# Kernel tuning notes

Measured on AMD Instinct MI355X. Metric: run time of the kernel, lower is better.

## Reference

```python
import jax, jax.numpy as jnp
import numpy as np

NUM_EMBEDDINGS = 1024
EMBEDDING_DIM = 256
COMMITMENT_COST = 0.25


def setup_inputs() -> dict:
    key = jax.random.key(0)
    kz, kc = jax.random.split(key)
    z = jax.random.normal(kz, (32, 32, 32, EMBEDDING_DIM), dtype=jnp.float32)
    # torch init: uniform(-1/K, 1/K)
    codebook = jax.random.uniform(
        kc, (NUM_EMBEDDINGS, EMBEDDING_DIM), dtype=jnp.float32,
        minval=-1.0 / NUM_EMBEDDINGS, maxval=1.0 / NUM_EMBEDDINGS)
    return {"z": z, "codebook": codebook}


def reference(z, codebook):
    K, D = codebook.shape
    zf = z.reshape(-1, D)                                   # [N, D]
    # squared L2 distances via expansion: ||z||^2 + ||e||^2 - 2 z.e
    distances = (jnp.sum(zf * zf, axis=1, keepdims=True)
                 + jnp.sum(codebook * codebook, axis=1)
                 - 2.0 * jnp.matmul(zf, codebook.T))        # [N, K]
    idx = jnp.argmin(distances, axis=1)                     # [N]
    encodings = jax.nn.one_hot(idx, K, dtype=z.dtype)       # [N, K]
    quantized = jnp.matmul(encodings, codebook).reshape(z.shape)
    e_latent_loss = jnp.mean((jax.lax.stop_gradient(quantized) - z) ** 2)
    q_latent_loss = jnp.mean((quantized - jax.lax.stop_gradient(z)) ** 2)
    loss = q_latent_loss + COMMITMENT_COST * e_latent_loss
    quantized_st = z + jax.lax.stop_gradient(quantized - z)  # straight-through
    return quantized_st, loss, encodings
```

## Files before the change

kernel.cpp:

```cpp
#include <hip/hip_runtime.h>

#define N_ROWS 32768
#define DIM 256
#define K_CODES 1024
#define KTOT 768
#define OUT_QUANT 8388608

typedef unsigned long long ull;
typedef _Float16 f16;
typedef __attribute__((ext_vector_type(4))) _Float16 f16x4;
typedef __attribute__((ext_vector_type(8))) _Float16 f16x8;
typedef __attribute__((ext_vector_type(4))) float f32x4;

#define NB_ZSPLIT 8192
#define NB_ZNORM 2048
#define NB_CSPLIT 256
#define NB_CNORM 64

struct HL { f16 h, l; };
__device__ __forceinline__ HL split2(float x) {
  f16 hh = (f16)x;
  if (__builtin_fabsf(x) < 6.103515625e-05f) hh = (f16)0.0f;
  const float r = __fsub_rn(x, (float)hh);
  HL o;
  o.h = hh;
  o.l = (f16)(__fmul_rn(r, 4096.0f));
  return o;
}

__global__ __launch_bounds__(256) void prep(
    const float* __restrict__ z, const float* __restrict__ cb,
    f16* __restrict__ Ap, f16* __restrict__ Bp,
    float* __restrict__ rn, float* __restrict__ cn,
    ull* __restrict__ keys, float* __restrict__ out) {
  const int b = blockIdx.x, tid = threadIdx.x;
  if (b < NB_ZSPLIT) {
    const size_t g = ((size_t)b * 256 + tid) * 4;
    const int row = (int)(g >> 8), k = (int)(g & 255);
    const float4 v = *(const float4*)(z + g);
    const HL s0 = split2(v.x), s1 = split2(v.y), s2 = split2(v.z), s3 = split2(v.w);
    const f16x4 h = {s0.h, s1.h, s2.h, s3.h};
    const f16x4 l = {s0.l, s1.l, s2.l, s3.l};
    f16* arow = Ap + (size_t)row * KTOT + k;
    *(f16x4*)(arow) = h;
    *(f16x4*)(arow + 256) = l;
    *(f16x4*)(arow + 512) = h;
  } else if (b < NB_ZSPLIT + NB_ZNORM) {
    const int row = (b - NB_ZSPLIT) * 16 + (tid >> 4);
    const int j = tid & 7, half = (tid >> 3) & 1;
    const float* x = z + (size_t)row * DIM + half * 128 + j;
    float r = __fmul_rn(x[0], x[0]);
#pragma unroll
    for (int t = 1; t < 16; ++t) r = __fadd_rn(r, __fmul_rn(x[8 * t], x[8 * t]));
    r = __fadd_rn(r, __shfl_xor(r, 1));
    r = __fadd_rn(r, __shfl_xor(r, 2));
    r = __fadd_rn(r, __shfl_xor(r, 4));
    const float o = __shfl_xor(r, 8);
    if ((tid & 15) == 0) {
      rn[row] = __fadd_rn(r, o);
      keys[row] = ~0ull;
    }
  } else if (b < NB_ZSPLIT + NB_ZNORM + NB_CSPLIT) {
    const int b2 = b - (NB_ZSPLIT + NB_ZNORM);
    const size_t g = ((size_t)b2 * 256 + tid) * 4;
    const int row = (int)(g >> 8), k = (int)(g & 255);
    const float4 v = *(const float4*)(cb + g);
    const HL s0 = split2(__fmul_rn(v.x, 1024.0f));
    const HL s1 = split2(__fmul_rn(v.y, 1024.0f));
    const HL s2 = split2(__fmul_rn(v.z, 1024.0f));
    const HL s3 = split2(__fmul_rn(v.w, 1024.0f));
    const f16x4 h = {s0.h, s1.h, s2.h, s3.h};
    const f16x4 l = {s0.l, s1.l, s2.l, s3.l};
    f16* brow = Bp + (size_t)row * KTOT + k;
    *(f16x4*)(brow) = h;
    *(f16x4*)(brow + 256) = h;
    *(f16x4*)(brow + 512) = l;
    if (b2 == 0 && tid == 0) out[OUT_QUANT] = 0.0f;
  } else {
    const int row = (b - (NB_ZSPLIT + NB_ZNORM + NB_CSPLIT)) * 16 + (tid >> 4);
    const int j = tid & 7, half = (tid >> 3) & 1;
    const float* x = cb + (size_t)row * DIM + half * 128 + j;
    float r = __fmul_rn(x[0], x[0]);
#pragma unroll
    for (int t = 1; t < 16; ++t) r = __fadd_rn(r, __fmul_rn(x[8 * t], x[8 * t]));
    r = __fadd_rn(r, __shfl_xor(r, 1));
    r = __fadd_rn(r, __shfl_xor(r, 2));
    r = __fadd_rn(r, __shfl_xor(r, 4));
    const float o = __shfl_xor(r, 8);
    if ((tid & 15) == 0) cn[row] = __fadd_rn(r, o);
  }
}

__device__ __forceinline__ void lds16(const void* g, void* l) {
  __builtin_amdgcn_global_load_lds(
      (const __attribute__((address_space(1))) unsigned int*)g,
      (__attribute__((address_space(3))) unsigned int*)l, 16, 0, 0);
}

__device__ __forceinline__ ull shflx64(ull v, int m) {
  int lo = __shfl_xor((int)(v & 0xffffffffull), m);
  int hi = __shfl_xor((int)(v >> 32), m);
  return ((ull)(unsigned int)hi << 32) | (unsigned int)lo;
}

__global__ __launch_bounds__(256) void gemm_argmin_f16(
    const f16* __restrict__ Ap, const f16* __restrict__ Bp,
    const float* __restrict__ rn, const float* __restrict__ cn,
    ull* __restrict__ keys) {
  __shared__ f16 As[2][4096];
  __shared__ f16 Bs[2][4096];

  const int bid = blockIdx.x;
  const int xcd = bid & 7, ii = bid >> 3;
  const int bm = xcd * 32 + (ii >> 3), bn = ii & 7;
  const int row0 = bm * 128, col0 = bn * 128;
  const int tid = threadIdx.x, wid = tid >> 6, lane = tid & 63;
  const int wm = wid >> 1, wn = wid & 1, lq = lane >> 4, lr = lane & 15;
  const int srow = tid & 127, shalf = tid >> 7;

  f32x4 acc[4][4];
#pragma unroll
  for (int a = 0; a < 4; ++a)
#pragma unroll
    for (int c = 0; c < 4; ++c) acc[a][c] = (f32x4){0.f, 0.f, 0.f, 0.f};

  const f16* aG = Ap + (size_t)(row0 + srow) * KTOT + shalf * 8;
  const f16* bG = Bp + (size_t)(col0 + srow) * KTOT + shalf * 8;

#pragma unroll
  for (int is = 0; is < 2; ++is) {
    lds16(aG + is * 16, (char*)As[0] + is * 4096 + tid * 16);
    lds16(bG + is * 16, (char*)Bs[0] + is * 4096 + tid * 16);
  }
  __syncthreads();

#pragma unroll
  for (int t = 0; t < 24; ++t) {
    const int cur = t & 1, nxt = cur ^ 1;
    if (t < 23) {
#pragma unroll
      for (int is = 0; is < 2; ++is) {
        lds16(aG + (t + 1) * 32 + is * 16, (char*)As[nxt] + is * 4096 + tid * 16);
        lds16(bG + (t + 1) * 32 + is * 16, (char*)Bs[nxt] + is * 4096 + tid * 16);
      }
    }
    if (t == 8) {
#pragma unroll
      for (int a = 0; a < 4; ++a)
#pragma unroll
        for (int c = 0; c < 4; ++c) acc[a][c] *= 4096.0f;
    }
    f16x8 av[4], bv[4];
    const f16x8* As8 = (const f16x8*)As[cur];
    const f16x8* Bs8 = (const f16x8*)Bs[cur];
#pragma unroll
    for (int fm = 0; fm < 4; ++fm) av[fm] = As8[lq * 128 + wm * 64 + fm * 16 + lr];
#pragma unroll
    for (int fn = 0; fn < 4; ++fn) bv[fn] = Bs8[lq * 128 + wn * 64 + fn * 16 + lr];
#pragma unroll
    for (int fm = 0; fm < 4; ++fm)
#pragma unroll
      for (int fn = 0; fn < 4; ++fn)
        acc[fm][fn] = __builtin_amdgcn_mfma_f32_16x16x32_f16(av[fm], bv[fn],
                                                             acc[fm][fn], 0, 0, 0);
    __syncthreads();
  }

  float cnv[4];
#pragma unroll
  for (int fn = 0; fn < 4; ++fn) cnv[fn] = cn[col0 + wn * 64 + fn * 16 + lr];

#pragma unroll
  for (int fm = 0; fm < 4; ++fm) {
#pragma unroll
    for (int j = 0; j < 4; ++j) {
      const int rg = row0 + wm * 64 + fm * 16 + lq * 4 + j;
      const float a_rn = rn[rg];
      ull best = ~0ull;
#pragma unroll
      for (int fn = 0; fn < 4; ++fn) {
        const int cg = col0 + wn * 64 + fn * 16 + lr;
        const float d = __fsub_rn(__fadd_rn(a_rn, cnv[fn]),
                                  __fmul_rn(acc[fm][fn][j], 4.76837158203125e-07f));
        unsigned int mono = __float_as_uint(d);
        mono = (mono & 0x80000000u) ? ~mono : (mono | 0x80000000u);
        const ull key = ((ull)mono << 32) | (unsigned int)cg;
        if (key < best) best = key;
      }
#pragma unroll
      for (int off = 1; off <= 8; off <<= 1) {
        ull o = shflx64(best, off);
        if (o < best) best = o;
      }
      if (lr == 0) atomicMin(&keys[rg], best);
    }
  }
}

__global__ __launch_bounds__(256) void quantize_out(
    const float* __restrict__ z, const float* __restrict__ cb,
    const ull* __restrict__ keys, float* __restrict__ out) {
  __shared__ float ls[4];
  const int wid = threadIdx.x >> 6, lane = threadIdx.x & 63;
  const int row = blockIdx.x * 4 + wid;
  const int idx = (int)(keys[row] & 0xffffffffull);
  const float4 zv = *(const float4*)(z + (size_t)row * DIM + lane * 4);
  const float4 qv = *(const float4*)(cb + (size_t)idx * DIM + lane * 4);
  const float dx = __fsub_rn(qv.x, zv.x);
  const float dy = __fsub_rn(qv.y, zv.y);
  const float dzz = __fsub_rn(qv.z, zv.z);
  const float dw = __fsub_rn(qv.w, zv.w);
  float4 ov;
  ov.x = __fadd_rn(zv.x, dx); ov.y = __fadd_rn(zv.y, dy);
  ov.z = __fadd_rn(zv.z, dzz); ov.w = __fadd_rn(zv.w, dw);
  *(float4*)(out + (size_t)row * DIM + lane * 4) = ov;
  float s = dx * dx + dy * dy + dzz * dzz + dw * dw;
#pragma unroll
  for (int o = 32; o > 0; o >>= 1) s += __shfl_down(s, o);
  if (lane == 0) ls[wid] = s;

  float4* enc4 = (float4*)(out + (size_t)OUT_QUANT + 1 + (size_t)row * K_CODES);
  const int target = idx >> 2, comp = idx & 3;
#pragma unroll
  for (int i = 0; i < 4; ++i) {
    const int f4i = lane + 64 * i;
    float4 v = {0.f, 0.f, 0.f, 0.f};
    if (f4i == target) ((float*)&v)[comp] = 1.0f;
    enc4[f4i] = v;
  }

  __syncthreads();
  if (threadIdx.x == 0)
    atomicAdd(out + OUT_QUANT, (ls[0] + ls[1] + ls[2] + ls[3]) * (1.25f / 8388608.0f));
}

extern "C" void kernel_launch(void* const* d_in, const int* in_sizes, int n_in,
                              void* d_out, int out_size, void* d_ws, size_t ws_size,
                              hipStream_t stream) {
  const float* z = (const float*)d_in[0];
  const float* cb = (const float*)d_in[1];
  float* out = (float*)d_out;

  char* w = (char*)d_ws;
  ull* keys = (ull*)w;
  float* rn = (float*)(w + (256u << 10));
  float* cn = (float*)(w + (384u << 10));
  f16* Ap = (f16*)(w + (512u << 10));
  f16* Bp = (f16*)(w + (512u << 10) + (48u << 20));

  prep<<<NB_ZSPLIT + NB_ZNORM + NB_CSPLIT + NB_CNORM, 256, 0, stream>>>(
      z, cb, Ap, Bp, rn, cn, keys, out);
  gemm_argmin_f16<<<2048, 256, 0, stream>>>(Ap, Bp, rn, cn, keys);
  quantize_out<<<N_ROWS / 4, 256, 0, stream>>>(z, cb, keys, out);
}
```

Baseline: 439.2 us.

## Drop LDS staging, load MFMA fragments directly from global with register pipelining

The GEMM-argmin kernel no longer stages A/B tiles through shared memory with global_load_lds and barriers. Each wave now owns a 64x64 tile and loads its MFMA fragments straight from global memory into a three-deep register ring, so no __syncthreads are needed. The A operand stores only the hi/lo halves (KA=512) and reuses the hi slice for the third K-segment by index remapping, which cuts prep writes and A-buffer size. The cost is that the four waves of a block no longer share loads, so there is more redundant global/L2 traffic, and the strided row loads may be less coalesced.

```diff
diff --git a/kernel.cpp b/kernel.cpp
--- a/kernel.cpp
+++ b/kernel.cpp
@@ -3,7 +3,8 @@
 #define N_ROWS 32768
 #define DIM 256
 #define K_CODES 1024
-#define KTOT 768
+#define KA 512
+#define KB 768
 #define OUT_QUANT 8388608
 
 typedef unsigned long long ull;
@@ -41,10 +42,9 @@
     const HL s0 = split2(v.x), s1 = split2(v.y), s2 = split2(v.z), s3 = split2(v.w);
     const f16x4 h = {s0.h, s1.h, s2.h, s3.h};
     const f16x4 l = {s0.l, s1.l, s2.l, s3.l};
-    f16* arow = Ap + (size_t)row * KTOT + k;
+    f16* arow = Ap + (size_t)row * KA + k;
     *(f16x4*)(arow) = h;
     *(f16x4*)(arow + 256) = l;
-    *(f16x4*)(arow + 512) = h;
   } else if (b < NB_ZSPLIT + NB_ZNORM) {
     const int row = (b - NB_ZSPLIT) * 16 + (tid >> 4);
     const int j = tid & 7, half = (tid >> 3) & 1;
@@ -71,10 +71,10 @@
     const HL s3 = split2(__fmul_rn(v.w, 1024.0f));
     const f16x4 h = {s0.h, s1.h, s2.h, s3.h};
     const f16x4 l = {s0.l, s1.l, s2.l, s3.l};
-    f16* brow = Bp + (size_t)row * KTOT + k;
+    f16* brow = Bp + (size_t)row * KB + k;
     *(f16x4*)(brow) = h;
-    *(f16x4*)(brow + 256) = h;
-    *(f16x4*)(brow + 512) = l;
+    *(f16x4*)(brow + 256) = l;
+    *(f16x4*)(brow + 512) = h;
     if (b2 == 0 && tid == 0) out[OUT_QUANT] = 0.0f;
   } else {
     const int row = (b - (NB_ZSPLIT + NB_ZNORM + NB_CSPLIT)) * 16 + (tid >> 4);
@@ -91,12 +91,6 @@
   }
 }
 
-__device__ __forceinline__ void lds16(const void* g, void* l) {
-  __builtin_amdgcn_global_load_lds(
-      (const __attribute__((address_space(1))) unsigned int*)g,
-      (__attribute__((address_space(3))) unsigned int*)l, 16, 0, 0);
-}
-
 __device__ __forceinline__ ull shflx64(ull v, int m) {
   int lo = __shfl_xor((int)(v & 0xffffffffull), m);
   int hi = __shfl_xor((int)(v >> 32), m);
@@ -107,16 +101,21 @@
     const f16* __restrict__ Ap, const f16* __restrict__ Bp,
     const float* __restrict__ rn, const float* __restrict__ cn,
     ull* __restrict__ keys) {
-  __shared__ f16 As[2][4096];
-  __shared__ f16 Bs[2][4096];
-
-  const int bid = blockIdx.x;
-  const int xcd = bid & 7, ii = bid >> 3;
-  const int bm = xcd * 32 + (ii >> 3), bn = ii & 7;
-  const int row0 = bm * 128, col0 = bn * 128;
-  const int tid = threadIdx.x, wid = tid >> 6, lane = tid & 63;
-  const int wm = wid >> 1, wn = wid & 1, lq = lane >> 4, lr = lane & 15;
-  const int srow = tid & 127, shalf = tid >> 7;
+  const int tid = threadIdx.x, w = tid >> 6, lane = tid & 63;
+  const int lq = lane >> 4, lr = lane & 15;
+  const int b = blockIdx.x;
+  const int xcd = b & 7, i = b >> 3;
+  const int mtile = xcd * 64 + (i >> 2);
+  const int ntile = (i & 3) * 4 + w;
+  const int row0 = mtile * 64, col0 = ntile * 64;
+
+  const f16* aR[4];
+  const f16* bR[4];
+#pragma unroll
+  for (int f = 0; f < 4; ++f) {
+    aR[f] = Ap + (size_t)(row0 + f * 16 + lr) * KA + lq * 8;
+    bR[f] = Bp + (size_t)(col0 + f * 16 + lr) * KB + lq * 8;
+  }
 
   f32x4 acc[4][4];
 #pragma unroll
@@ -124,24 +123,27 @@
 #pragma unroll
     for (int c = 0; c < 4; ++c) acc[a][c] = (f32x4){0.f, 0.f, 0.f, 0.f};
 
-  const f16* aG = Ap + (size_t)(row0 + srow) * KTOT + shalf * 8;
-  const f16* bG = Bp + (size_t)(col0 + srow) * KTOT + shalf * 8;
-
-#pragma unroll
-  for (int is = 0; is < 2; ++is) {
-    lds16(aG + is * 16, (char*)As[0] + is * 4096 + tid * 16);
-    lds16(bG + is * 16, (char*)Bs[0] + is * 4096 + tid * 16);
-  }
-  __syncthreads();
+  f16x8 av[3][4], bv[3][4];
+#pragma unroll
+  for (int p = 0; p < 2; ++p) {
+    const int ao = (p < 8 ? p : p - 8) * 32, bo = p * 32;
+#pragma unroll
+    for (int f = 0; f < 4; ++f) {
+      av[p][f] = *(const f16x8*)(aR[f] + ao);
+      bv[p][f] = *(const f16x8*)(bR[f] + bo);
+    }
+  }
 
 #pragma unroll
   for (int t = 0; t < 24; ++t) {
-    const int cur = t & 1, nxt = cur ^ 1;
-    if (t < 23) {
-#pragma unroll
-      for (int is = 0; is < 2; ++is) {
-        lds16(aG + (t + 1) * 32 + is * 16, (char*)As[nxt] + is * 4096 + tid * 16);
-        lds16(bG + (t + 1) * 32 + is * 16, (char*)Bs[nxt] + is * 4096 + tid * 16);
+    const int cur = t % 3;
+    if (t < 22) {
+      const int nxt = (t + 2) % 3, tt = t + 2;
+      const int ao = (tt < 8 ? tt : tt - 8) * 32, bo = tt * 32;
+#pragma unroll
+      for (int f = 0; f < 4; ++f) {
+        av[nxt][f] = *(const f16x8*)(aR[f] + ao);
+        bv[nxt][f] = *(const f16x8*)(bR[f] + bo);
       }
     }
     if (t == 8) {
@@ -150,36 +152,28 @@
 #pragma unroll
         for (int c = 0; c < 4; ++c) acc[a][c] *= 4096.0f;
     }
-    f16x8 av[4], bv[4];
-    const f16x8* As8 = (const f16x8*)As[cur];
-    const f16x8* Bs8 = (const f16x8*)Bs[cur];
-#pragma unroll
-    for (int fm = 0; fm < 4; ++fm) av[fm] = As8[lq * 128 + wm * 64 + fm * 16 + lr];
-#pragma unroll
-    for (int fn = 0; fn < 4; ++fn) bv[fn] = Bs8[lq * 128 + wn * 64 + fn * 16 + lr];
 #pragma unroll
     for (int fm = 0; fm < 4; ++fm)
 #pragma unroll
       for (int fn = 0; fn < 4; ++fn)
-        acc[fm][fn] = __builtin_amdgcn_mfma_f32_16x16x32_f16(av[fm], bv[fn],
+        acc[fm][fn] = __builtin_amdgcn_mfma_f32_16x16x32_f16(av[cur][fm], bv[cur][fn],
                                                              acc[fm][fn], 0, 0, 0);
-    __syncthreads();
   }
 
   float cnv[4];
 #pragma unroll
-  for (int fn = 0; fn < 4; ++fn) cnv[fn] = cn[col0 + wn * 64 + fn * 16 + lr];
+  for (int fn = 0; fn < 4; ++fn) cnv[fn] = cn[col0 + fn * 16 + lr];
 
 #pragma unroll
   for (int fm = 0; fm < 4; ++fm) {
 #pragma unroll
     for (int j = 0; j < 4; ++j) {
-      const int rg = row0 + wm * 64 + fm * 16 + lq * 4 + j;
+      const int rg = row0 + fm * 16 + lq * 4 + j;
       const float a_rn = rn[rg];
       ull best = ~0ull;
 #pragma unroll
       for (int fn = 0; fn < 4; ++fn) {
-        const int cg = col0 + wn * 64 + fn * 16 + lr;
+        const int cg = col0 + fn * 16 + lr;
         const float d = __fsub_rn(__fadd_rn(a_rn, cnv[fn]),
                                   __fmul_rn(acc[fm][fn][j], 4.76837158203125e-07f));
         unsigned int mono = __float_as_uint(d);
@@ -246,7 +240,7 @@
   float* rn = (float*)(w + (256u << 10));
   float* cn = (float*)(w + (384u << 10));
   f16* Ap = (f16*)(w + (512u << 10));
-  f16* Bp = (f16*)(w + (512u << 10) + (48u << 20));
+  f16* Bp = (f16*)(w + (512u << 10) + (32u << 20));
 
   prep<<<NB_ZSPLIT + NB_ZNORM + NB_CSPLIT + NB_CNORM, 256, 0, stream>>>(
       z, cb, Ap, Bp, rn, cn, keys, out);
```

New measurement: 460.1 us. +4.8%, slower.
